# Kernel tuning notes

Measured on AMD Instinct MI355X. Metric: run time of the kernel, lower is better.

Reference implementation:

```python
import jax, jax.numpy as jnp
import numpy as np

N_HEADS = 16
NEG_BIAS = -1000000000.0


def setup_inputs() -> dict:
    key = jax.random.key(0)
    k1, k2, k3, k4 = jax.random.split(key, 4)
    B, S, D = 2, 2048, 1024
    queries = jax.random.normal(k1, (B, S, D), dtype=jnp.float32)
    keys = jax.random.normal(k2, (B, S, D), dtype=jnp.float32)
    values = jax.random.normal(k3, (B, S, D), dtype=jnp.float32)
    mask = jax.random.randint(k4, (B, S, S), 0, 2, dtype=jnp.int32)
    return {"queries": queries, "keys": keys, "values": values, "mask": mask}


def _split_heads(x):
    B, S, D = x.shape
    return x.reshape(B, S, N_HEADS, D // N_HEADS).transpose(0, 2, 1, 3)  # [B,H,S,d]


def reference(queries, keys, values, mask):
    q = _split_heads(queries)   # [B,H,Sq,d]
    k = _split_heads(keys)      # [B,H,Sk,d]
    v = _split_heads(values)    # [B,H,Sk,d]
    d_head = q.shape[-1]
    # scaled dot product similarity
    sim = jnp.einsum('bhqd,bhkd->bhqk', q, k) / jnp.sqrt(jnp.float32(d_head))
    # additive mask (softmax attention function -> non-hadamard)
    bias = NEG_BIAS * (1.0 - mask.astype(sim.dtype))[:, None]  # [B,1,Sq,Sk]
    sim = sim + bias
    # softmax with max-subtraction (numerically stable, as in original)
    weights = jax.nn.softmax(sim, axis=-1)
    out = jnp.einsum('bhqk,bhkd->bhqd', weights, v)  # [B,H,Sq,d]
    B, H, Sq, d = out.shape
    return out.transpose(0, 2, 1, 3).reshape(B, Sq, H * d)
```

## Files before the change

kernel.cpp:

```cpp
#include <hip/hip_runtime.h>

#define S_LEN 2048
#define D_MODEL 1024
#define DH 64
#define BQ 128
#define BK 128
#define LDK 72
#define LDV 136
#define ZSCALE 0.18033688f
#define M0F    12.0f
#define ZBIAS  -1.5e9f

using short8 = __attribute__((ext_vector_type(8))) short;
using s4v    = __attribute__((ext_vector_type(4))) short;
using f32x4  = __attribute__((ext_vector_type(4))) float;

__device__ __forceinline__ unsigned short f2bf(float x) {
    union { float f; unsigned int u; } c; c.f = x;
    unsigned int u = c.u;
    u += 0x7fffu + ((u >> 16) & 1u);
    return (unsigned short)(u >> 16);
}

__global__ __launch_bounds__(256) void cvt_fused(const float* __restrict__ V,
                                                 const int* __restrict__ M,
                                                 const float* __restrict__ K,
                                                 unsigned short* __restrict__ VT,
                                                 unsigned long long* __restrict__ Mb,
                                                 unsigned short* __restrict__ KB) {
    const int blk = blockIdx.x;
    const int tid = threadIdx.x;
    if (blk < 1024) {
        __shared__ float tsF[64][65];
        const int b  = blk >> 9;
        const int h  = (blk >> 5) & 15;
        const int s0 = (blk & 31) * 64;
        #pragma unroll
        for (int it = 0; it < 2; ++it) {
            int seg = tid + it * 256;
            int s = seg >> 3, d8 = (seg & 7) << 3;
            const float* p = V + (size_t)(b * S_LEN + s0 + s) * D_MODEL + h * DH + d8;
            f32x4 a = *(const f32x4*)p;
            f32x4 c = *(const f32x4*)(p + 4);
            #pragma unroll
            for (int j = 0; j < 4; ++j) { tsF[s][d8 + j] = a[j]; tsF[s][d8 + 4 + j] = c[j]; }
        }
        __syncthreads();
        #pragma unroll
        for (int it = 0; it < 2; ++it) {
            int seg = tid + it * 256;
            int d = seg >> 3, s8 = (seg & 7) << 3;
            short8 w;
            #pragma unroll
            for (int j = 0; j < 8; ++j) w[j] = (short)f2bf(tsF[s8 + j][d]);
            *(short8*)(VT + ((size_t)((b * 16 + h) * 64 + d)) * S_LEN + s0 + s8) = w;
        }
    } else if (blk < 2048) {
        const int pb   = blk - 1024;
        const int wave = tid >> 6, lane = tid & 63;
        const int row  = pb * 4 + wave;
        const int* mp  = M + (size_t)row * S_LEN;
        #pragma unroll 4
        for (int it = 0; it < 32; ++it) {
            int m = mp[it * 64 + lane];
            unsigned long long bal = __ballot(m != 0);
            if (lane == 0) Mb[(size_t)row * 32 + it] = bal;
        }
    } else {
        size_t base = (size_t)(blk - 2048) * 4096;
        #pragma unroll
        for (int it = 0; it < 4; ++it) {
            size_t i = base + ((size_t)(it * 256 + tid)) * 4;
            f32x4 a = *(const f32x4*)(K + i);
            s4v w;
            #pragma unroll
            for (int j = 0; j < 4; ++j) w[j] = (short)f2bf(a[j]);
            *(s4v*)(KB + i) = w;
        }
    }
}

__global__ __launch_bounds__(256) void mha_fwd_v7(
    const float* __restrict__ Q,
    const float* __restrict__ K,
    const unsigned short* __restrict__ KB,
    const unsigned short* __restrict__ VT,
    const unsigned long long* __restrict__ Mb,
    float* __restrict__ O,
    int kbf)
{
    __shared__ alignas(16) unsigned short Ks[BK][LDK];
    __shared__ alignas(16) unsigned short Vt[DH][LDV];

    const int blk0 = blockIdx.x;
    const int blk  = ((blk0 & 7) << 6) | (blk0 >> 3);

    const int b   = blk >> 8;
    const int h   = (blk >> 4) & 15;
    const int qbase = (blk & 15) * BQ;
    const int bh  = b * 16 + h;

    const int tid  = threadIdx.x;
    const int wave = tid >> 6;
    const int lane = tid & 63;
    const int n16  = lane & 15;
    const int quad = lane >> 4;
    const int bq   = quad << 3;

    const int srow = tid >> 3, sc8 = (tid & 7) << 3;
    const int prow = (((srow >> 2) & 1) << 4) | (((srow >> 3) & 3) << 2) | (srow & 3);
    const int vrow = tid >> 4, vc8 = (tid & 15) << 3;

    short8 qf[2][2];
    #pragma unroll
    for (int qg = 0; qg < 2; ++qg) {
        const size_t qoff = (size_t)(b * S_LEN + qbase + wave * 32 + qg * 16 + n16) * D_MODEL
                          + h * DH + quad * 8;
        f32x4 a0 = *(const f32x4*)(Q + qoff);
        f32x4 a1 = *(const f32x4*)(Q + qoff + 4);
        f32x4 a2 = *(const f32x4*)(Q + qoff + 32);
        f32x4 a3 = *(const f32x4*)(Q + qoff + 36);
        short8 q0, q1;
        #pragma unroll
        for (int j = 0; j < 4; ++j) {
            q0[j] = (short)f2bf(a0[j]); q0[4 + j] = (short)f2bf(a1[j]);
            q1[j] = (short)f2bf(a2[j]); q1[4 + j] = (short)f2bf(a3[j]);
        }
        qf[qg][0] = q0; qf[qg][1] = q1;
    }

    const short8 ones = {0x3F80,0x3F80,0x3F80,0x3F80,0x3F80,0x3F80,0x3F80,0x3F80};

    f32x4 o[2][4], o4[2];
    #pragma unroll
    for (int qg = 0; qg < 2; ++qg) {
        #pragma unroll
        for (int dg = 0; dg < 4; ++dg) o[qg][dg] = f32x4{0.f,0.f,0.f,0.f};
        o4[qg] = f32x4{0.f,0.f,0.f,0.f};
    }

    const unsigned long long* mrow[2];
    #pragma unroll
    for (int qg = 0; qg < 2; ++qg)
        mrow[qg] = Mb + (size_t)(b * S_LEN + qbase + wave * 32 + qg * 16 + n16) * 32;

    const size_t kbase = (size_t)(b * S_LEN) * D_MODEL + h * DH;
    const size_t vbase = (size_t)(bh * 64) * S_LEN;

    short8 ka[4], va[4];
    unsigned long long mw[2][2];
    if (kbf) {
        #pragma unroll
        for (int i = 0; i < 4; ++i)
            ka[i] = *(const short8*)(KB + kbase + (size_t)(i * 32 + srow) * D_MODEL + sc8);
    } else {
        #pragma unroll
        for (int i = 0; i < 4; ++i) {
            const float* kp = K + kbase + (size_t)(i * 32 + srow) * D_MODEL + sc8;
            f32x4 p0 = *(const f32x4*)kp, p1 = *(const f32x4*)(kp + 4);
            short8 w;
            #pragma unroll
            for (int j = 0; j < 4; ++j) { w[j] = (short)f2bf(p0[j]); w[4 + j] = (short)f2bf(p1[j]); }
            ka[i] = w;
        }
    }
    #pragma unroll
    for (int i = 0; i < 4; ++i)
        va[i] = *(const short8*)(VT + vbase + (size_t)(vrow + 16 * i) * S_LEN + vc8);
    #pragma unroll
    for (int qg = 0; qg < 2; ++qg) { mw[qg][0] = mrow[qg][0]; mw[qg][1] = mrow[qg][1]; }

    for (int kb = 0; kb < S_LEN; kb += BK) {
        __syncthreads();
        #pragma unroll
        for (int i = 0; i < 4; ++i) {
            *(short8*)&Ks[prow + 32 * i][sc8] = ka[i];
            *(short8*)&Vt[vrow + 16 * i][vc8] = va[i];
        }

        const int kn = kb + BK;
        const bool more = kn < S_LEN;
        short8 nka[4], nva[4];
        unsigned long long nmw[2][2];
        if (more) {
            if (kbf) {
                #pragma unroll
                for (int i = 0; i < 4; ++i)
                    nka[i] = *(const short8*)(KB + kbase + (size_t)(kn + i * 32 + srow) * D_MODEL + sc8);
            } else {
                #pragma unroll
                for (int i = 0; i < 4; ++i) {
                    const float* kp = K + kbase + (size_t)(kn + i * 32 + srow) * D_MODEL + sc8;
                    f32x4 p0 = *(const f32x4*)kp, p1 = *(const f32x4*)(kp + 4);
                    short8 w;
                    #pragma unroll
                    for (int j = 0; j < 4; ++j) { w[j] = (short)f2bf(p0[j]); w[4 + j] = (short)f2bf(p1[j]); }
                    nka[i] = w;
                }
            }
            #pragma unroll
            for (int i = 0; i < 4; ++i)
                nva[i] = *(const short8*)(VT + vbase + (size_t)(vrow + 16 * i) * S_LEN + kn + vc8);
            const int wi = kn >> 6;
            #pragma unroll
            for (int qg = 0; qg < 2; ++qg) { nmw[qg][0] = mrow[qg][wi]; nmw[qg][1] = mrow[qg][wi + 1]; }
        }
        __syncthreads();

        unsigned int am[2][4];
        #pragma unroll
        for (int qg = 0; qg < 2; ++qg) {
            am[qg][0] = ((unsigned int)mw[qg][0]) >> bq;
            am[qg][1] = ((unsigned int)(mw[qg][0] >> 32)) >> bq;
            am[qg][2] = ((unsigned int)mw[qg][1]) >> bq;
            am[qg][3] = ((unsigned int)(mw[qg][1] >> 32)) >> bq;
        }

        union { unsigned int u[4]; short8 v; } Af[2][4];
        __builtin_amdgcn_s_setprio(1);
        #pragma unroll
        for (int ct = 0; ct < 8; ++ct) {
            short8 kf0 = *(const short8*)&Ks[ct * 16 + n16][     quad * 8];
            short8 kf1 = *(const short8*)&Ks[ct * 16 + n16][32 + quad * 8];
            f32x4 sA = {0.f,0.f,0.f,0.f}, sB = sA;
            sA = __builtin_amdgcn_mfma_f32_16x16x32_bf16(kf0, qf[0][0], sA, 0, 0, 0);
            sA = __builtin_amdgcn_mfma_f32_16x16x32_bf16(kf1, qf[0][1], sA, 0, 0, 0);
            sB = __builtin_amdgcn_mfma_f32_16x16x32_bf16(kf0, qf[1][0], sB, 0, 0, 0);
            sB = __builtin_amdgcn_mfma_f32_16x16x32_bf16(kf1, qf[1][1], sB, 0, 0, 0);
            const int sel = ct >> 1, sb = (ct & 1) * 4;
            unsigned int puA[4], puB[4];
            #pragma unroll
            for (int r = 0; r < 4; ++r) {
                float zA = fmaf(sA[r], ZSCALE, ((am[0][sel] >> (sb + r)) & 1u) ? -M0F : ZBIAS);
                float zB = fmaf(sB[r], ZSCALE, ((am[1][sel] >> (sb + r)) & 1u) ? -M0F : ZBIAS);
                puA[r] = __float_as_uint(__builtin_amdgcn_exp2f(zA));
                puB[r] = __float_as_uint(__builtin_amdgcn_exp2f(zB));
            }
            const int kc = ct >> 1, ub = (ct & 1) * 2;
            Af[0][kc].u[ub + 0] = __builtin_amdgcn_perm(puA[1], puA[0], 0x07060302);
            Af[0][kc].u[ub + 1] = __builtin_amdgcn_perm(puA[3], puA[2], 0x07060302);
            Af[1][kc].u[ub + 0] = __builtin_amdgcn_perm(puB[1], puB[0], 0x07060302);
            Af[1][kc].u[ub + 1] = __builtin_amdgcn_perm(puB[3], puB[2], 0x07060302);
        }

        #pragma unroll
        for (int kc = 0; kc < 4; ++kc) {
            short8 v0 = *(const short8*)&Vt[      n16][kc * 32 + quad * 8];
            short8 v1 = *(const short8*)&Vt[16 + n16][kc * 32 + quad * 8];
            short8 v2 = *(const short8*)&Vt[32 + n16][kc * 32 + quad * 8];
            short8 v3 = *(const short8*)&Vt[48 + n16][kc * 32 + quad * 8];
            #pragma unroll
            for (int qg = 0; qg < 2; ++qg) {
                short8 af = Af[qg][kc].v;
                o[qg][0] = __builtin_amdgcn_mfma_f32_16x16x32_bf16(af, v0, o[qg][0], 0, 0, 0);
                o[qg][1] = __builtin_amdgcn_mfma_f32_16x16x32_bf16(af, v1, o[qg][1], 0, 0, 0);
                o[qg][2] = __builtin_amdgcn_mfma_f32_16x16x32_bf16(af, v2, o[qg][2], 0, 0, 0);
                o[qg][3] = __builtin_amdgcn_mfma_f32_16x16x32_bf16(af, v3, o[qg][3], 0, 0, 0);
                o4[qg]   = __builtin_amdgcn_mfma_f32_16x16x32_bf16(af, ones, o4[qg], 0, 0, 0);
            }
        }
        __builtin_amdgcn_s_setprio(0);

        if (more) {
            #pragma unroll
            for (int i = 0; i < 4; ++i) { ka[i] = nka[i]; va[i] = nva[i]; }
            #pragma unroll
            for (int qg = 0; qg < 2; ++qg) { mw[qg][0] = nmw[qg][0]; mw[qg][1] = nmw[qg][1]; }
        }
    }

    #pragma unroll
    for (int qg = 0; qg < 2; ++qg) {
        #pragma unroll
        for (int r = 0; r < 4; ++r) {
            float rl = 1.f / o4[qg][r];
            size_t row = (size_t)(b * S_LEN + qbase + wave * 32 + qg * 16 + quad * 4 + r);
            float* op = O + row * D_MODEL + h * DH + n16;
            op[0]  = o[qg][0][r] * rl;
            op[16] = o[qg][1][r] * rl;
            op[32] = o[qg][2][r] * rl;
            op[48] = o[qg][3][r] * rl;
        }
    }
}

extern "C" void kernel_launch(void* const* d_in, const int* in_sizes, int n_in,
                              void* d_out, int out_size, void* d_ws, size_t ws_size,
                              hipStream_t stream) {
    const float* Q = (const float*)d_in[0];
    const float* K = (const float*)d_in[1];
    const float* V = (const float*)d_in[2];
    const int*   M = (const int*)d_in[3];
    float*       O = (float*)d_out;

    const size_t NEL = (size_t)2 * S_LEN * D_MODEL;
    const size_t VT_BYTES = NEL * sizeof(unsigned short);
    const size_t KB_BYTES = NEL * sizeof(unsigned short);
    const size_t MB_BYTES = (size_t)2 * S_LEN * 32 * 8;

    if (ws_size >= VT_BYTES + KB_BYTES + MB_BYTES) {
        unsigned short* VT = (unsigned short*)d_ws;
        unsigned short* KB = (unsigned short*)((char*)d_ws + VT_BYTES);
        unsigned long long* Mb = (unsigned long long*)((char*)d_ws + VT_BYTES + KB_BYTES);
        hipLaunchKernelGGL(cvt_fused, dim3(3072), dim3(256), 0, stream, V, M, K, VT, Mb, KB);
        hipLaunchKernelGGL(mha_fwd_v7, dim3(512), dim3(256), 0, stream,
                           Q, K, KB, VT, Mb, O, 1);
    } else {
        unsigned short* VT = (unsigned short*)d_ws;
        unsigned long long* Mb = (unsigned long long*)((char*)d_ws + VT_BYTES);
        hipLaunchKernelGGL(cvt_fused, dim3(2048), dim3(256), 0, stream, V, M, K, VT, Mb, (unsigned short*)0);
        hipLaunchKernelGGL(mha_fwd_v7, dim3(512), dim3(256), 0, stream,
                           Q, K, (const unsigned short*)0, VT, Mb, O, 0);
    }
}
```

Measured before the change: 175.4 us.

## Drop LDS staging; load K and V MFMA fragments directly from global memory

Removes the shared-memory tiles for K and transposed V, along with the register double-buffering and both __syncthreads per key block. Each wave now loads its K and V MFMA operands straight from global memory, using a permuted row index that keeps the previous fragment layout. This drops LDS writes, LDS reads and block-wide barriers. In exchange, the four waves each fetch the same K/V data redundantly through the cache, and the loads are no longer prefetched one iteration ahead, so global latency may be exposed. The setprio regions are also narrowed around the MFMA groups.

```diff
diff --git a/kernel.cpp b/kernel.cpp
--- a/kernel.cpp
+++ b/kernel.cpp
@@ -5,8 +5,6 @@
 #define DH 64
 #define BQ 128
 #define BK 128
-#define LDK 72
-#define LDV 136
 #define ZSCALE 0.18033688f
 #define M0F    12.0f
 #define ZBIAS  -1.5e9f
@@ -80,7 +78,7 @@
     }
 }
 
-__global__ __launch_bounds__(256) void mha_fwd_v7(
+__global__ __launch_bounds__(256) void mha_fwd_v8(
     const float* __restrict__ Q,
     const float* __restrict__ K,
     const unsigned short* __restrict__ KB,
@@ -89,9 +87,6 @@
     float* __restrict__ O,
     int kbf)
 {
-    __shared__ alignas(16) unsigned short Ks[BK][LDK];
-    __shared__ alignas(16) unsigned short Vt[DH][LDV];
-
     const int blk0 = blockIdx.x;
     const int blk  = ((blk0 & 7) << 6) | (blk0 >> 3);
 
@@ -106,10 +101,7 @@
     const int n16  = lane & 15;
     const int quad = lane >> 4;
     const int bq   = quad << 3;
-
-    const int srow = tid >> 3, sc8 = (tid & 7) << 3;
-    const int prow = (((srow >> 2) & 1) << 4) | (((srow >> 3) & 3) << 2) | (srow & 3);
-    const int vrow = tid >> 4, vc8 = (tid & 15) << 3;
+    const int lrow = ((n16 >> 2) << 3) | (n16 & 3);
 
     short8 qf[2][2];
     #pragma unroll
@@ -146,87 +138,45 @@
 
     const size_t kbase = (size_t)(b * S_LEN) * D_MODEL + h * DH;
     const size_t vbase = (size_t)(bh * 64) * S_LEN;
-
-    short8 ka[4], va[4];
-    unsigned long long mw[2][2];
-    if (kbf) {
-        #pragma unroll
-        for (int i = 0; i < 4; ++i)
-            ka[i] = *(const short8*)(KB + kbase + (size_t)(i * 32 + srow) * D_MODEL + sc8);
-    } else {
-        #pragma unroll
-        for (int i = 0; i < 4; ++i) {
-            const float* kp = K + kbase + (size_t)(i * 32 + srow) * D_MODEL + sc8;
-            f32x4 p0 = *(const f32x4*)kp, p1 = *(const f32x4*)(kp + 4);
-            short8 w;
-            #pragma unroll
-            for (int j = 0; j < 4; ++j) { w[j] = (short)f2bf(p0[j]); w[4 + j] = (short)f2bf(p1[j]); }
-            ka[i] = w;
-        }
-    }
-    #pragma unroll
-    for (int i = 0; i < 4; ++i)
-        va[i] = *(const short8*)(VT + vbase + (size_t)(vrow + 16 * i) * S_LEN + vc8);
-    #pragma unroll
-    for (int qg = 0; qg < 2; ++qg) { mw[qg][0] = mrow[qg][0]; mw[qg][1] = mrow[qg][1]; }
+    const unsigned short* vtp = VT + vbase + quad * 8;
 
     for (int kb = 0; kb < S_LEN; kb += BK) {
-        __syncthreads();
-        #pragma unroll
-        for (int i = 0; i < 4; ++i) {
-            *(short8*)&Ks[prow + 32 * i][sc8] = ka[i];
-            *(short8*)&Vt[vrow + 16 * i][vc8] = va[i];
-        }
-
-        const int kn = kb + BK;
-        const bool more = kn < S_LEN;
-        short8 nka[4], nva[4];
-        unsigned long long nmw[2][2];
-        if (more) {
+        const int wi = kb >> 6;
+        unsigned long long mwA0 = mrow[0][wi], mwA1 = mrow[0][wi + 1];
+        unsigned long long mwB0 = mrow[1][wi], mwB1 = mrow[1][wi + 1];
+        unsigned int am[2][4];
+        am[0][0] = ((unsigned int)mwA0) >> bq;  am[0][1] = ((unsigned int)(mwA0 >> 32)) >> bq;
+        am[0][2] = ((unsigned int)mwA1) >> bq;  am[0][3] = ((unsigned int)(mwA1 >> 32)) >> bq;
+        am[1][0] = ((unsigned int)mwB0) >> bq;  am[1][1] = ((unsigned int)(mwB0 >> 32)) >> bq;
+        am[1][2] = ((unsigned int)mwB1) >> bq;  am[1][3] = ((unsigned int)(mwB1 >> 32)) >> bq;
+
+        union { unsigned int u[4]; short8 v; } Af[2][4];
+        #pragma unroll
+        for (int ct = 0; ct < 8; ++ct) {
+            const int cst  = ((ct >> 2) << 6) | (((ct >> 1) & 1) << 5) | ((ct & 1) << 2);
+            const int crow = kb + cst + lrow;
+            short8 kf0, kf1;
             if (kbf) {
+                const unsigned short* kp = KB + kbase + (size_t)crow * D_MODEL + quad * 8;
+                kf0 = *(const short8*)kp;
+                kf1 = *(const short8*)(kp + 32);
+            } else {
+                const float* kp = K + kbase + (size_t)crow * D_MODEL + quad * 8;
+                f32x4 p0 = *(const f32x4*)kp,        p1 = *(const f32x4*)(kp + 4);
+                f32x4 p2 = *(const f32x4*)(kp + 32), p3 = *(const f32x4*)(kp + 36);
                 #pragma unroll
-                for (int i = 0; i < 4; ++i)
-                    nka[i] = *(const short8*)(KB + kbase + (size_t)(kn + i * 32 + srow) * D_MODEL + sc8);
-            } else {
-                #pragma unroll
-                for (int i = 0; i < 4; ++i) {
-                    const float* kp = K + kbase + (size_t)(kn + i * 32 + srow) * D_MODEL + sc8;
-                    f32x4 p0 = *(const f32x4*)kp, p1 = *(const f32x4*)(kp + 4);
-                    short8 w;
-                    #pragma unroll
-                    for (int j = 0; j < 4; ++j) { w[j] = (short)f2bf(p0[j]); w[4 + j] = (short)f2bf(p1[j]); }
-                    nka[i] = w;
+                for (int j = 0; j < 4; ++j) {
+                    kf0[j] = (short)f2bf(p0[j]); kf0[4 + j] = (short)f2bf(p1[j]);
+                    kf1[j] = (short)f2bf(p2[j]); kf1[4 + j] = (short)f2bf(p3[j]);
                 }
             }
-            #pragma unroll
-            for (int i = 0; i < 4; ++i)
-                nva[i] = *(const short8*)(VT + vbase + (size_t)(vrow + 16 * i) * S_LEN + kn + vc8);
-            const int wi = kn >> 6;
-            #pragma unroll
-            for (int qg = 0; qg < 2; ++qg) { nmw[qg][0] = mrow[qg][wi]; nmw[qg][1] = mrow[qg][wi + 1]; }
-        }
-        __syncthreads();
-
-        unsigned int am[2][4];
-        #pragma unroll
-        for (int qg = 0; qg < 2; ++qg) {
-            am[qg][0] = ((unsigned int)mw[qg][0]) >> bq;
-            am[qg][1] = ((unsigned int)(mw[qg][0] >> 32)) >> bq;
-            am[qg][2] = ((unsigned int)mw[qg][1]) >> bq;
-            am[qg][3] = ((unsigned int)(mw[qg][1] >> 32)) >> bq;
-        }
-
-        union { unsigned int u[4]; short8 v; } Af[2][4];
-        __builtin_amdgcn_s_setprio(1);
-        #pragma unroll
-        for (int ct = 0; ct < 8; ++ct) {
-            short8 kf0 = *(const short8*)&Ks[ct * 16 + n16][     quad * 8];
-            short8 kf1 = *(const short8*)&Ks[ct * 16 + n16][32 + quad * 8];
+            __builtin_amdgcn_s_setprio(1);
             f32x4 sA = {0.f,0.f,0.f,0.f}, sB = sA;
             sA = __builtin_amdgcn_mfma_f32_16x16x32_bf16(kf0, qf[0][0], sA, 0, 0, 0);
             sA = __builtin_amdgcn_mfma_f32_16x16x32_bf16(kf1, qf[0][1], sA, 0, 0, 0);
             sB = __builtin_amdgcn_mfma_f32_16x16x32_bf16(kf0, qf[1][0], sB, 0, 0, 0);
             sB = __builtin_amdgcn_mfma_f32_16x16x32_bf16(kf1, qf[1][1], sB, 0, 0, 0);
+            __builtin_amdgcn_s_setprio(0);
             const int sel = ct >> 1, sb = (ct & 1) * 4;
             unsigned int puA[4], puB[4];
             #pragma unroll
@@ -243,12 +193,14 @@
             Af[1][kc].u[ub + 1] = __builtin_amdgcn_perm(puB[3], puB[2], 0x07060302);
         }
 
+        __builtin_amdgcn_s_setprio(1);
         #pragma unroll
         for (int kc = 0; kc < 4; ++kc) {
-            short8 v0 = *(const short8*)&Vt[      n16][kc * 32 + quad * 8];
-            short8 v1 = *(const short8*)&Vt[16 + n16][kc * 32 + quad * 8];
-            short8 v2 = *(const short8*)&Vt[32 + n16][kc * 32 + quad * 8];
-            short8 v3 = *(const short8*)&Vt[48 + n16][kc * 32 + quad * 8];
+            const unsigned short* vp = vtp + kb + kc * 32;
+            short8 v0 = *(const short8*)(vp + (size_t)(      n16) * S_LEN);
+            short8 v1 = *(const short8*)(vp + (size_t)(16 + n16) * S_LEN);
+            short8 v2 = *(const short8*)(vp + (size_t)(32 + n16) * S_LEN);
+            short8 v3 = *(const short8*)(vp + (size_t)(48 + n16) * S_LEN);
             #pragma unroll
             for (int qg = 0; qg < 2; ++qg) {
                 short8 af = Af[qg][kc].v;
@@ -260,13 +212,6 @@
             }
         }
         __builtin_amdgcn_s_setprio(0);
-
-        if (more) {
-            #pragma unroll
-            for (int i = 0; i < 4; ++i) { ka[i] = nka[i]; va[i] = nva[i]; }
-            #pragma unroll
-            for (int qg = 0; qg < 2; ++qg) { mw[qg][0] = nmw[qg][0]; mw[qg][1] = nmw[qg][1]; }
-        }
     }
 
     #pragma unroll
@@ -303,13 +248,13 @@
         unsigned short* KB = (unsigned short*)((char*)d_ws + VT_BYTES);
         unsigned long long* Mb = (unsigned long long*)((char*)d_ws + VT_BYTES + KB_BYTES);
         hipLaunchKernelGGL(cvt_fused, dim3(3072), dim3(256), 0, stream, V, M, K, VT, Mb, KB);
-        hipLaunchKernelGGL(mha_fwd_v7, dim3(512), dim3(256), 0, stream,
+        hipLaunchKernelGGL(mha_fwd_v8, dim3(512), dim3(256), 0, stream,
                            Q, K, KB, VT, Mb, O, 1);
     } else {
         unsigned short* VT = (unsigned short*)d_ws;
         unsigned long long* Mb = (unsigned long long*)((char*)d_ws + VT_BYTES);
         hipLaunchKernelGGL(cvt_fused, dim3(2048), dim3(256), 0, stream, V, M, K, VT, Mb, (unsigned short*)0);
-        hipLaunchKernelGGL(mha_fwd_v7, dim3(512), dim3(256), 0, stream,
+        hipLaunchKernelGGL(mha_fwd_v8, dim3(512), dim3(256), 0, stream,
                            Q, K, (const unsigned short*)0, VT, Mb, O, 0);
     }
 }
```

Result: slower. 248.2 us (+41.5%).

## Load V fragments directly from global memory and double-buffer K in LDS

Applied to the files above, without the earlier changes.

V tiles are no longer staged through shared memory. Each wave loads its MFMA B-operand fragments straight from the pre-transposed bf16 VT buffer into registers. K shared memory becomes double-buffered, so one barrier per iteration replaces two. This removes the LDS writes and reads for V and a sync point. The cost is that each of the four waves now fetches the same V data from global or L2 memory, register pressure grows with 16 short8 fragments, and the V loads are issued in the same iteration they are used, so their latency is less hidden.

```diff
diff --git a/kernel.cpp b/kernel.cpp
--- a/kernel.cpp
+++ b/kernel.cpp
@@ -6,7 +6,6 @@
 #define BQ 128
 #define BK 128
 #define LDK 72
-#define LDV 136
 #define ZSCALE 0.18033688f
 #define M0F    12.0f
 #define ZBIAS  -1.5e9f
@@ -80,7 +79,7 @@
     }
 }
 
-__global__ __launch_bounds__(256) void mha_fwd_v7(
+__global__ __launch_bounds__(256) void mha_fwd_v9(
     const float* __restrict__ Q,
     const float* __restrict__ K,
     const unsigned short* __restrict__ KB,
@@ -89,8 +88,7 @@
     float* __restrict__ O,
     int kbf)
 {
-    __shared__ alignas(16) unsigned short Ks[BK][LDK];
-    __shared__ alignas(16) unsigned short Vt[DH][LDV];
+    __shared__ alignas(16) unsigned short Ks[2][BK][LDK];
 
     const int blk0 = blockIdx.x;
     const int blk  = ((blk0 & 7) << 6) | (blk0 >> 3);
@@ -109,7 +107,6 @@
 
     const int srow = tid >> 3, sc8 = (tid & 7) << 3;
     const int prow = (((srow >> 2) & 1) << 4) | (((srow >> 3) & 3) << 2) | (srow & 3);
-    const int vrow = tid >> 4, vc8 = (tid & 15) << 3;
 
     short8 qf[2][2];
     #pragma unroll
@@ -146,8 +143,12 @@
 
     const size_t kbase = (size_t)(b * S_LEN) * D_MODEL + h * DH;
     const size_t vbase = (size_t)(bh * 64) * S_LEN;
-
-    short8 ka[4], va[4];
+    const unsigned short* vrp[4];
+    #pragma unroll
+    for (int dg = 0; dg < 4; ++dg)
+        vrp[dg] = VT + vbase + (size_t)(16 * dg + n16) * S_LEN + quad * 8;
+
+    short8 ka[4];
     unsigned long long mw[2][2];
     if (kbf) {
         #pragma unroll
@@ -165,22 +166,25 @@
         }
     }
     #pragma unroll
-    for (int i = 0; i < 4; ++i)
-        va[i] = *(const short8*)(VT + vbase + (size_t)(vrow + 16 * i) * S_LEN + vc8);
-    #pragma unroll
     for (int qg = 0; qg < 2; ++qg) { mw[qg][0] = mrow[qg][0]; mw[qg][1] = mrow[qg][1]; }
 
-    for (int kb = 0; kb < S_LEN; kb += BK) {
-        __syncthreads();
-        #pragma unroll
-        for (int i = 0; i < 4; ++i) {
-            *(short8*)&Ks[prow + 32 * i][sc8] = ka[i];
-            *(short8*)&Vt[vrow + 16 * i][vc8] = va[i];
-        }
+    int p = 0;
+    #pragma unroll 2
+    for (int kb = 0; kb < S_LEN; kb += BK, p ^= 1) {
+        #pragma unroll
+        for (int i = 0; i < 4; ++i)
+            *(short8*)&Ks[p][prow + 32 * i][sc8] = ka[i];
+
+        short8 vf[4][4];
+        #pragma unroll
+        for (int dg = 0; dg < 4; ++dg)
+            #pragma unroll
+            for (int kc = 0; kc < 4; ++kc)
+                vf[dg][kc] = *(const short8*)(vrp[dg] + kb + kc * 32);
 
         const int kn = kb + BK;
         const bool more = kn < S_LEN;
-        short8 nka[4], nva[4];
+        short8 nka[4];
         unsigned long long nmw[2][2];
         if (more) {
             if (kbf) {
@@ -198,14 +202,14 @@
                     nka[i] = w;
                 }
             }
-            #pragma unroll
-            for (int i = 0; i < 4; ++i)
-                nva[i] = *(const short8*)(VT + vbase + (size_t)(vrow + 16 * i) * S_LEN + kn + vc8);
             const int wi = kn >> 6;
             #pragma unroll
             for (int qg = 0; qg < 2; ++qg) { nmw[qg][0] = mrow[qg][wi]; nmw[qg][1] = mrow[qg][wi + 1]; }
         }
-        __syncthreads();
+
+        asm volatile("s_waitcnt lgkmcnt(0)" ::: "memory");
+        __builtin_amdgcn_s_barrier();
+        __builtin_amdgcn_sched_barrier(0);
 
         unsigned int am[2][4];
         #pragma unroll
@@ -220,8 +224,8 @@
         __builtin_amdgcn_s_setprio(1);
         #pragma unroll
         for (int ct = 0; ct < 8; ++ct) {
-            short8 kf0 = *(const short8*)&Ks[ct * 16 + n16][     quad * 8];
-            short8 kf1 = *(const short8*)&Ks[ct * 16 + n16][32 + quad * 8];
+            short8 kf0 = *(const short8*)&Ks[p][ct * 16 + n16][     quad * 8];
+            short8 kf1 = *(const short8*)&Ks[p][ct * 16 + n16][32 + quad * 8];
             f32x4 sA = {0.f,0.f,0.f,0.f}, sB = sA;
             sA = __builtin_amdgcn_mfma_f32_16x16x32_bf16(kf0, qf[0][0], sA, 0, 0, 0);
             sA = __builtin_amdgcn_mfma_f32_16x16x32_bf16(kf1, qf[0][1], sA, 0, 0, 0);
@@ -245,17 +249,13 @@
 
         #pragma unroll
         for (int kc = 0; kc < 4; ++kc) {
-            short8 v0 = *(const short8*)&Vt[      n16][kc * 32 + quad * 8];
-            short8 v1 = *(const short8*)&Vt[16 + n16][kc * 32 + quad * 8];
-            short8 v2 = *(const short8*)&Vt[32 + n16][kc * 32 + quad * 8];
-            short8 v3 = *(const short8*)&Vt[48 + n16][kc * 32 + quad * 8];
             #pragma unroll
             for (int qg = 0; qg < 2; ++qg) {
                 short8 af = Af[qg][kc].v;
-                o[qg][0] = __builtin_amdgcn_mfma_f32_16x16x32_bf16(af, v0, o[qg][0], 0, 0, 0);
-                o[qg][1] = __builtin_amdgcn_mfma_f32_16x16x32_bf16(af, v1, o[qg][1], 0, 0, 0);
-                o[qg][2] = __builtin_amdgcn_mfma_f32_16x16x32_bf16(af, v2, o[qg][2], 0, 0, 0);
-                o[qg][3] = __builtin_amdgcn_mfma_f32_16x16x32_bf16(af, v3, o[qg][3], 0, 0, 0);
+                o[qg][0] = __builtin_amdgcn_mfma_f32_16x16x32_bf16(af, vf[0][kc], o[qg][0], 0, 0, 0);
+                o[qg][1] = __builtin_amdgcn_mfma_f32_16x16x32_bf16(af, vf[1][kc], o[qg][1], 0, 0, 0);
+                o[qg][2] = __builtin_amdgcn_mfma_f32_16x16x32_bf16(af, vf[2][kc], o[qg][2], 0, 0, 0);
+                o[qg][3] = __builtin_amdgcn_mfma_f32_16x16x32_bf16(af, vf[3][kc], o[qg][3], 0, 0, 0);
                 o4[qg]   = __builtin_amdgcn_mfma_f32_16x16x32_bf16(af, ones, o4[qg], 0, 0, 0);
             }
         }
@@ -263,7 +263,7 @@
 
         if (more) {
             #pragma unroll
-            for (int i = 0; i < 4; ++i) { ka[i] = nka[i]; va[i] = nva[i]; }
+            for (int i = 0; i < 4; ++i) ka[i] = nka[i];
             #pragma unroll
             for (int qg = 0; qg < 2; ++qg) { mw[qg][0] = nmw[qg][0]; mw[qg][1] = nmw[qg][1]; }
         }
@@ -303,13 +303,13 @@
         unsigned short* KB = (unsigned short*)((char*)d_ws + VT_BYTES);
         unsigned long long* Mb = (unsigned long long*)((char*)d_ws + VT_BYTES + KB_BYTES);
         hipLaunchKernelGGL(cvt_fused, dim3(3072), dim3(256), 0, stream, V, M, K, VT, Mb, KB);
-        hipLaunchKernelGGL(mha_fwd_v7, dim3(512), dim3(256), 0, stream,
+        hipLaunchKernelGGL(mha_fwd_v9, dim3(512), dim3(256), 0, stream,
                            Q, K, KB, VT, Mb, O, 1);
     } else {
         unsigned short* VT = (unsigned short*)d_ws;
         unsigned long long* Mb = (unsigned long long*)((char*)d_ws + VT_BYTES);
         hipLaunchKernelGGL(cvt_fused, dim3(2048), dim3(256), 0, stream, V, M, K, VT, Mb, (unsigned short*)0);
-        hipLaunchKernelGGL(mha_fwd_v7, dim3(512), dim3(256), 0, stream,
+        hipLaunchKernelGGL(mha_fwd_v9, dim3(512), dim3(256), 0, stream,
                            Q, K, (const unsigned short*)0, VT, Mb, O, 0);
     }
 }
```

Result: slower. 199.9 us (+14.0%).

## Pre-expand mask into MFMA-fragment layout and apply it with bitwise AND

Applied to the files above, without the earlier changes.

The mask is no longer packed into a bitmask. The prep kernel now expands it into a 16-bit (or 8-bit fallback) all-ones/all-zeros word per element, stored in the exact order of the attention kernel's P fragments. Inside the attention loop, masking becomes an AND on the packed bf16 probabilities, and the softmax scale is folded into Q during its bf16 conversion, so the per-element fmaf, bit extraction and select are gone. The cost is much larger mask data: a 16 MB expanded mask is written every call and re-read by all 16 heads of each batch, instead of a 1 MB bitmask. The constant exp offset is also dropped, which relies on scores staying in a safe range.

```diff
diff --git a/kernel.cpp b/kernel.cpp
--- a/kernel.cpp
+++ b/kernel.cpp
@@ -8,12 +8,11 @@
 #define LDK 72
 #define LDV 136
 #define ZSCALE 0.18033688f
-#define M0F    12.0f
-#define ZBIAS  -1.5e9f
 
 using short8 = __attribute__((ext_vector_type(8))) short;
 using s4v    = __attribute__((ext_vector_type(4))) short;
 using f32x4  = __attribute__((ext_vector_type(4))) float;
+using int4v  = __attribute__((ext_vector_type(4))) int;
 
 __device__ __forceinline__ unsigned short f2bf(float x) {
     union { float f; unsigned int u; } c; c.f = x;
@@ -26,7 +25,8 @@
                                                  const int* __restrict__ M,
                                                  const float* __restrict__ K,
                                                  unsigned short* __restrict__ VT,
-                                                 unsigned long long* __restrict__ Mb,
+                                                 unsigned short* __restrict__ EM16,
+                                                 unsigned char* __restrict__ EMB,
                                                  unsigned short* __restrict__ KB) {
     const int blk = blockIdx.x;
     const int tid = threadIdx.x;
@@ -56,15 +56,39 @@
             *(short8*)(VT + ((size_t)((b * 16 + h) * 64 + d)) * S_LEN + s0 + s8) = w;
         }
     } else if (blk < 2048) {
-        const int pb   = blk - 1024;
-        const int wave = tid >> 6, lane = tid & 63;
-        const int row  = pb * 4 + wave;
-        const int* mp  = M + (size_t)row * S_LEN;
-        #pragma unroll 4
-        for (int it = 0; it < 32; ++it) {
-            int m = mp[it * 64 + lane];
-            unsigned long long bal = __ballot(m != 0);
-            if (lane == 0) Mb[(size_t)row * 32 + it] = bal;
+        const unsigned int pb = blk - 1024;
+        #pragma unroll
+        for (int it = 0; it < 4; ++it) {
+            unsigned int c = (pb << 10) | (it << 8) | (unsigned int)tid;
+            const int lane = c & 63;
+            const int kc   = (c >> 6) & 3;
+            const int qg   = (c >> 8) & 1;
+            const int w    = (c >> 9) & 3;
+            const int kt   = (c >> 11) & 15;
+            const int qt   = (c >> 15) & 15;
+            const int bb   = (c >> 19) & 1;
+            const int q    = qt * 128 + w * 32 + qg * 16 + (lane & 15);
+            const int k0   = kt * 128 + ((kc >> 1) << 6) + ((kc & 1) << 5) + ((lane >> 4) << 3);
+            const int* mp  = M + (((size_t)(bb * S_LEN + q)) << 11) + k0;
+            int4v a = *(const int4v*)mp;
+            int4v d = *(const int4v*)(mp + 4);
+            if (EM16) {
+                short8 wv;
+                #pragma unroll
+                for (int j = 0; j < 4; ++j) {
+                    wv[j]     = (short)(a[j] ? 0xFFFF : 0);
+                    wv[4 + j] = (short)(d[j] ? 0xFFFF : 0);
+                }
+                *(short8*)(EM16 + (size_t)c * 8) = wv;
+            } else {
+                unsigned long long v = 0;
+                #pragma unroll
+                for (int j = 0; j < 4; ++j) {
+                    if (a[j]) v |= 0xFFull << (8 * j);
+                    if (d[j]) v |= 0xFFull << (8 * (4 + j));
+                }
+                *(unsigned long long*)(EMB + (size_t)c * 8) = v;
+            }
         }
     } else {
         size_t base = (size_t)(blk - 2048) * 4096;
@@ -80,14 +104,15 @@
     }
 }
 
-__global__ __launch_bounds__(256) void mha_fwd_v7(
+__global__ __launch_bounds__(256) void mha_fwd_v10(
     const float* __restrict__ Q,
     const float* __restrict__ K,
     const unsigned short* __restrict__ KB,
     const unsigned short* __restrict__ VT,
-    const unsigned long long* __restrict__ Mb,
+    const unsigned short* __restrict__ EM16,
+    const unsigned char* __restrict__ EMB,
     float* __restrict__ O,
-    int kbf)
+    int kbf, int em16)
 {
     __shared__ alignas(16) unsigned short Ks[BK][LDK];
     __shared__ alignas(16) unsigned short Vt[DH][LDV];
@@ -97,7 +122,8 @@
 
     const int b   = blk >> 8;
     const int h   = (blk >> 4) & 15;
-    const int qbase = (blk & 15) * BQ;
+    const int qt  = blk & 15;
+    const int qbase = qt * BQ;
     const int bh  = b * 16 + h;
 
     const int tid  = threadIdx.x;
@@ -105,7 +131,6 @@
     const int lane = tid & 63;
     const int n16  = lane & 15;
     const int quad = lane >> 4;
-    const int bq   = quad << 3;
 
     const int srow = tid >> 3, sc8 = (tid & 7) << 3;
     const int prow = (((srow >> 2) & 1) << 4) | (((srow >> 3) & 3) << 2) | (srow & 3);
@@ -123,8 +148,8 @@
         short8 q0, q1;
         #pragma unroll
         for (int j = 0; j < 4; ++j) {
-            q0[j] = (short)f2bf(a0[j]); q0[4 + j] = (short)f2bf(a1[j]);
-            q1[j] = (short)f2bf(a2[j]); q1[4 + j] = (short)f2bf(a3[j]);
+            q0[j] = (short)f2bf(a0[j] * ZSCALE); q0[4 + j] = (short)f2bf(a1[j] * ZSCALE);
+            q1[j] = (short)f2bf(a2[j] * ZSCALE); q1[4 + j] = (short)f2bf(a3[j] * ZSCALE);
         }
         qf[qg][0] = q0; qf[qg][1] = q1;
     }
@@ -139,16 +164,12 @@
         o4[qg] = f32x4{0.f,0.f,0.f,0.f};
     }
 
-    const unsigned long long* mrow[2];
-    #pragma unroll
-    for (int qg = 0; qg < 2; ++qg)
-        mrow[qg] = Mb + (size_t)(b * S_LEN + qbase + wave * 32 + qg * 16 + n16) * 32;
-
     const size_t kbase = (size_t)(b * S_LEN) * D_MODEL + h * DH;
     const size_t vbase = (size_t)(bh * 64) * S_LEN;
+    const size_t embase = ((size_t)((b << 4) + qt) << 18) + ((size_t)wave << 12)
+                        + ((size_t)lane << 3);
 
     short8 ka[4], va[4];
-    unsigned long long mw[2][2];
     if (kbf) {
         #pragma unroll
         for (int i = 0; i < 4; ++i)
@@ -167,8 +188,6 @@
     #pragma unroll
     for (int i = 0; i < 4; ++i)
         va[i] = *(const short8*)(VT + vbase + (size_t)(vrow + 16 * i) * S_LEN + vc8);
-    #pragma unroll
-    for (int qg = 0; qg < 2; ++qg) { mw[qg][0] = mrow[qg][0]; mw[qg][1] = mrow[qg][1]; }
 
     for (int kb = 0; kb < S_LEN; kb += BK) {
         __syncthreads();
@@ -178,10 +197,26 @@
             *(short8*)&Vt[vrow + 16 * i][vc8] = va[i];
         }
 
+        const size_t emoff = embase + ((size_t)(kb >> 7) << 14);
+        union { short8 v; unsigned int u[4]; } emf[2][4];
+        unsigned long long emb[2][4];
+        if (em16) {
+            #pragma unroll
+            for (int qg = 0; qg < 2; ++qg)
+                #pragma unroll
+                for (int kc = 0; kc < 4; ++kc)
+                    emf[qg][kc].v = *(const short8*)(EM16 + emoff + (qg << 11) + (kc << 9));
+        } else {
+            #pragma unroll
+            for (int qg = 0; qg < 2; ++qg)
+                #pragma unroll
+                for (int kc = 0; kc < 4; ++kc)
+                    emb[qg][kc] = *(const unsigned long long*)(EMB + emoff + (qg << 11) + (kc << 9));
+        }
+
         const int kn = kb + BK;
         const bool more = kn < S_LEN;
         short8 nka[4], nva[4];
-        unsigned long long nmw[2][2];
         if (more) {
             if (kbf) {
                 #pragma unroll
@@ -201,20 +236,8 @@
             #pragma unroll
             for (int i = 0; i < 4; ++i)
                 nva[i] = *(const short8*)(VT + vbase + (size_t)(vrow + 16 * i) * S_LEN + kn + vc8);
-            const int wi = kn >> 6;
-            #pragma unroll
-            for (int qg = 0; qg < 2; ++qg) { nmw[qg][0] = mrow[qg][wi]; nmw[qg][1] = mrow[qg][wi + 1]; }
         }
         __syncthreads();
-
-        unsigned int am[2][4];
-        #pragma unroll
-        for (int qg = 0; qg < 2; ++qg) {
-            am[qg][0] = ((unsigned int)mw[qg][0]) >> bq;
-            am[qg][1] = ((unsigned int)(mw[qg][0] >> 32)) >> bq;
-            am[qg][2] = ((unsigned int)mw[qg][1]) >> bq;
-            am[qg][3] = ((unsigned int)(mw[qg][1] >> 32)) >> bq;
-        }
 
         union { unsigned int u[4]; short8 v; } Af[2][4];
         __builtin_amdgcn_s_setprio(1);
@@ -227,20 +250,29 @@
             sA = __builtin_amdgcn_mfma_f32_16x16x32_bf16(kf1, qf[0][1], sA, 0, 0, 0);
             sB = __builtin_amdgcn_mfma_f32_16x16x32_bf16(kf0, qf[1][0], sB, 0, 0, 0);
             sB = __builtin_amdgcn_mfma_f32_16x16x32_bf16(kf1, qf[1][1], sB, 0, 0, 0);
-            const int sel = ct >> 1, sb = (ct & 1) * 4;
             unsigned int puA[4], puB[4];
             #pragma unroll
             for (int r = 0; r < 4; ++r) {
-                float zA = fmaf(sA[r], ZSCALE, ((am[0][sel] >> (sb + r)) & 1u) ? -M0F : ZBIAS);
-                float zB = fmaf(sB[r], ZSCALE, ((am[1][sel] >> (sb + r)) & 1u) ? -M0F : ZBIAS);
-                puA[r] = __float_as_uint(__builtin_amdgcn_exp2f(zA));
-                puB[r] = __float_as_uint(__builtin_amdgcn_exp2f(zB));
+                puA[r] = __float_as_uint(__builtin_amdgcn_exp2f(sA[r]));
+                puB[r] = __float_as_uint(__builtin_amdgcn_exp2f(sB[r]));
             }
             const int kc = ct >> 1, ub = (ct & 1) * 2;
-            Af[0][kc].u[ub + 0] = __builtin_amdgcn_perm(puA[1], puA[0], 0x07060302);
-            Af[0][kc].u[ub + 1] = __builtin_amdgcn_perm(puA[3], puA[2], 0x07060302);
-            Af[1][kc].u[ub + 0] = __builtin_amdgcn_perm(puB[1], puB[0], 0x07060302);
-            Af[1][kc].u[ub + 1] = __builtin_amdgcn_perm(puB[3], puB[2], 0x07060302);
+            unsigned int mA0, mA1, mB0, mB1;
+            if (em16) {
+                mA0 = emf[0][kc].u[ub];  mA1 = emf[0][kc].u[ub + 1];
+                mB0 = emf[1][kc].u[ub];  mB1 = emf[1][kc].u[ub + 1];
+            } else {
+                unsigned int hA = (ub == 0) ? (unsigned int)emb[0][kc] : (unsigned int)(emb[0][kc] >> 32);
+                unsigned int hB = (ub == 0) ? (unsigned int)emb[1][kc] : (unsigned int)(emb[1][kc] >> 32);
+                mA0 = __builtin_amdgcn_perm(0u, hA, 0x01010000u);
+                mA1 = __builtin_amdgcn_perm(0u, hA, 0x03030202u);
+                mB0 = __builtin_amdgcn_perm(0u, hB, 0x01010000u);
+                mB1 = __builtin_amdgcn_perm(0u, hB, 0x03030202u);
+            }
+            Af[0][kc].u[ub + 0] = __builtin_amdgcn_perm(puA[1], puA[0], 0x07060302u) & mA0;
+            Af[0][kc].u[ub + 1] = __builtin_amdgcn_perm(puA[3], puA[2], 0x07060302u) & mA1;
+            Af[1][kc].u[ub + 0] = __builtin_amdgcn_perm(puB[1], puB[0], 0x07060302u) & mB0;
+            Af[1][kc].u[ub + 1] = __builtin_amdgcn_perm(puB[3], puB[2], 0x07060302u) & mB1;
         }
 
         #pragma unroll
@@ -264,8 +296,6 @@
         if (more) {
             #pragma unroll
             for (int i = 0; i < 4; ++i) { ka[i] = nka[i]; va[i] = nva[i]; }
-            #pragma unroll
-            for (int qg = 0; qg < 2; ++qg) { mw[qg][0] = nmw[qg][0]; mw[qg][1] = nmw[qg][1]; }
         }
     }
 
@@ -294,22 +324,25 @@
     float*       O = (float*)d_out;
 
     const size_t NEL = (size_t)2 * S_LEN * D_MODEL;
-    const size_t VT_BYTES = NEL * sizeof(unsigned short);
-    const size_t KB_BYTES = NEL * sizeof(unsigned short);
-    const size_t MB_BYTES = (size_t)2 * S_LEN * 32 * 8;
-
-    if (ws_size >= VT_BYTES + KB_BYTES + MB_BYTES) {
+    const size_t VT_BYTES  = NEL * sizeof(unsigned short);
+    const size_t KB_BYTES  = NEL * sizeof(unsigned short);
+    const size_t EM16_BYTES = (size_t)2 * S_LEN * S_LEN * 2;
+    const size_t EMB_BYTES  = (size_t)2 * S_LEN * S_LEN;
+
+    if (ws_size >= VT_BYTES + KB_BYTES + EM16_BYTES) {
         unsigned short* VT = (unsigned short*)d_ws;
         unsigned short* KB = (unsigned short*)((char*)d_ws + VT_BYTES);
-        unsigned long long* Mb = (unsigned long long*)((char*)d_ws + VT_BYTES + KB_BYTES);
-        hipLaunchKernelGGL(cvt_fused, dim3(3072), dim3(256), 0, stream, V, M, K, VT, Mb, KB);
-        hipLaunchKernelGGL(mha_fwd_v7, dim3(512), dim3(256), 0, stream,
-                           Q, K, KB, VT, Mb, O, 1);
+        unsigned short* EM = (unsigned short*)((char*)d_ws + VT_BYTES + KB_BYTES);
+        hipLaunchKernelGGL(cvt_fused, dim3(3072), dim3(256), 0, stream,
+                           V, M, K, VT, EM, (unsigned char*)0, KB);
+        hipLaunchKernelGGL(mha_fwd_v10, dim3(512), dim3(256), 0, stream,
+                           Q, K, KB, VT, EM, (const unsigned char*)0, O, 1, 1);
     } else {
         unsigned short* VT = (unsigned short*)d_ws;
-        unsigned long long* Mb = (unsigned long long*)((char*)d_ws + VT_BYTES);
-        hipLaunchKernelGGL(cvt_fused, dim3(2048), dim3(256), 0, stream, V, M, K, VT, Mb, (unsigned short*)0);
-        hipLaunchKernelGGL(mha_fwd_v7, dim3(512), dim3(256), 0, stream,
-                           Q, K, (const unsigned short*)0, VT, Mb, O, 0);
+        unsigned char*  EB = (unsigned char*)((char*)d_ws + VT_BYTES);
+        hipLaunchKernelGGL(cvt_fused, dim3(2048), dim3(256), 0, stream,
+                           V, M, K, VT, (unsigned short*)0, EB, (unsigned short*)0);
+        hipLaunchKernelGGL(mha_fwd_v10, dim3(512), dim3(256), 0, stream,
+                           Q, K, (const unsigned short*)0, VT, (const unsigned short*)0, EB, O, 0, 0);
     }
 }
```

After: 207.1 us. +18.1%, slower.
